# Kernel optimization log

Measured on AMD Instinct MI355X. Metric: run time of the kernel, lower is better.

The kernel has to match this reference:

```python
import jax, jax.numpy as jnp
import numpy as np

HIDDEN_DIM = 2048
HEAD_NUM = 16
HEAD_DIM = HIDDEN_DIM // HEAD_NUM


def setup_inputs() -> dict:
    key = jax.random.key(0)
    ks = jax.random.split(key, 9)
    B, S, H = 2, 2048, HIDDEN_DIM
    scale = 1.0 / np.sqrt(H)
    X = jax.random.normal(ks[0], (B, S, H), dtype=jnp.float32)
    Wq = jax.random.normal(ks[1], (H, H), dtype=jnp.float32) * scale
    bq = jnp.zeros((H,), dtype=jnp.float32)
    Wk = jax.random.normal(ks[2], (H, H), dtype=jnp.float32) * scale
    bk = jnp.zeros((H,), dtype=jnp.float32)
    Wv = jax.random.normal(ks[3], (H, H), dtype=jnp.float32) * scale
    bv = jnp.zeros((H,), dtype=jnp.float32)
    Wo = jax.random.normal(ks[4], (H, H), dtype=jnp.float32) * scale
    bo = jnp.zeros((H,), dtype=jnp.float32)
    return {"X": X, "Wq": Wq, "bq": bq, "Wk": Wk, "bk": bk,
            "Wv": Wv, "bv": bv, "Wo": Wo, "bo": bo}


def reference(X, Wq, bq, Wk, bk, Wv, bv, Wo, bo):
    B, S, H = X.shape
    # QKV projections (nn.Linear applies x @ W.T + b; weights here stored as [in, out])
    Q = X @ Wq + bq
    K = X @ Wk + bk
    V = X @ Wv + bv
    # [B, heads, S, head_dim]
    q = Q.reshape(B, S, HEAD_NUM, HEAD_DIM).transpose(0, 2, 1, 3)
    k = K.reshape(B, S, HEAD_NUM, HEAD_DIM).transpose(0, 2, 1, 3)
    v = V.reshape(B, S, HEAD_NUM, HEAD_DIM).transpose(0, 2, 1, 3)
    scores = jnp.einsum('bhqd,bhkd->bhqk', q, k) / jnp.sqrt(jnp.float32(HEAD_DIM))
    attn = jax.nn.softmax(scores, axis=-1)  # dropout = identity in eval
    out = jnp.einsum('bhqk,bhkd->bhqd', attn, v)
    out = out.transpose(0, 2, 1, 3).reshape(B, S, H)
    return out @ Wo + bo
```

## Files before the change

### kernel.cpp

```cpp
#include <hip/hip_runtime.h>
#include <hip/hip_bf16.h>
#include <stdint.h>


#define Bc 2
#define Sc 2048
#define Hc 2048
#define NHc 16
#define Dc 128
#define Mc 4096

typedef unsigned short ushortT;
typedef float f32x4 __attribute__((ext_vector_type(4)));
typedef _Float16 f16x8 __attribute__((ext_vector_type(8)));

#define MFMAH(a, b, c) __builtin_amdgcn_mfma_f32_16x16x32_f16((a), (b), (c), 0, 0, 0)

static __device__ __forceinline__ ushortT f2h(float x) {
    _Float16 h = (_Float16)x;
    return __builtin_bit_cast(unsigned short, h);
}

static __device__ __forceinline__ void load_lds16(const ushortT* g, ushortT* l) {
    __builtin_amdgcn_global_load_lds(
        (__attribute__((address_space(1))) void*)(g),
        (__attribute__((address_space(3))) void*)(l), 16, 0, 0);
}

__global__ __launch_bounds__(256) void pack_a(
    const float* __restrict__ src, ushortT* __restrict__ dst)
{
    const int mt = blockIdx.x, kt = blockIdx.y;
    const int t = threadIdx.x;
    const int kq = t & 15;
    const int r0 = t >> 4;
    ushortT* tile = dst + ((size_t)(mt * 32 + kt)) * 8192;
#pragma unroll
    for (int rr = 0; rr < 8; ++rr) {
        const int row = r0 + rr * 16;
        const float4 v = *(const float4*)(src + (size_t)(mt * 128 + row) * Hc + kt * 64 + kq * 4);
        _Float16 h[4] = {(_Float16)v.x, (_Float16)v.y, (_Float16)v.z, (_Float16)v.w};
        const int gid = kq >> 1, halfg = kq & 1;
        const int gp = gid ^ (row & 7);
        *(uint2*)(tile + (size_t)row * 64 + gp * 8 + halfg * 4) = *(uint2*)h;
    }
}

__global__ __launch_bounds__(256) void pack_b(
    const float* __restrict__ W0, const float* __restrict__ W1,
    const float* __restrict__ W2, const float* __restrict__ W3,
    ushortT* __restrict__ dst)
{
    const int nt = blockIdx.x, kt = blockIdx.y, which = blockIdx.z;
    const float* W = (which == 0) ? W0 : (which == 1) ? W1 : (which == 2) ? W2 : W3;
    const int t = threadIdx.x;
    const int n = t & 127;
    const int g0 = (t >> 7) * 4;
    ushortT* tile = dst + (size_t)which * 4194304 + ((size_t)(nt * 32 + kt)) * 8192;
#pragma unroll
    for (int gi = 0; gi < 4; ++gi) {
        const int g = g0 + gi;
        _Float16 h[8];
#pragma unroll
        for (int j = 0; j < 8; ++j)
            h[j] = (_Float16)W[(size_t)(kt * 64 + g * 8 + j) * Hc + nt * 128 + n];
        const int gp = g ^ (n & 7);
        *(uint4*)(tile + (size_t)n * 64 + gp * 8) = *(uint4*)h;
    }
}

#define GEMM_PROLOGUE()                                                        \
    __shared__ __align__(16) ushortT As[8192], Bs[8192];                       \
    const int tid = threadIdx.x, wv_ = tid >> 6, lane = tid & 63;              \
    const int lane16 = lane & 15, quad = lane >> 4;                            \
    const int quad4 = quad * 4;                                                \
    const int wm = (wv_ & 1) * 64, wn = (wv_ >> 1) * 64;                       \
    int aoff[4][2], boff[4][2];                                                \
    _Pragma("unroll") for (int mi = 0; mi < 4; ++mi)                           \
        _Pragma("unroll") for (int kf = 0; kf < 2; ++kf) {                     \
            const int ra = wm + mi * 16 + lane16;                              \
            aoff[mi][kf] = ra * 64 + (((kf * 4 + quad) ^ (ra & 7)) << 3);      \
            const int rb = wn + mi * 16 + lane16;                              \
            boff[mi][kf] = rb * 64 + (((kf * 4 + quad) ^ (rb & 7)) << 3);      \
        }                                                                      \
    f32x4 acc[4][4];                                                           \
    _Pragma("unroll") for (int i = 0; i < 4; ++i)                              \
        _Pragma("unroll") for (int j = 0; j < 4; ++j) {                        \
            acc[i][j][0] = 0.f; acc[i][j][1] = 0.f;                            \
            acc[i][j][2] = 0.f; acc[i][j][3] = 0.f; }                          \
    ushortT* asd = &As[wv_ * 2048];                                            \
    ushortT* bsd = &Bs[wv_ * 2048];

#define GEMM_KLOOP(at, bt)                                                     \
    for (int kt2 = 0; kt2 < 32; ++kt2) {                                       \
        _Pragma("unroll") for (int i = 0; i < 4; ++i) {                        \
            load_lds16(at + i * 512 + lane * 8, asd + i * 512);                \
            load_lds16(bt + i * 512 + lane * 8, bsd + i * 512);                \
        }                                                                      \
        at += 8192; bt += 8192;                                                \
        __syncthreads();                                                       \
        _Pragma("unroll") for (int kf = 0; kf < 2; ++kf) {                     \
            f16x8 a[4], b[4];                                                  \
            _Pragma("unroll") for (int mi = 0; mi < 4; ++mi)                   \
                a[mi] = *(const f16x8*)&As[aoff[mi][kf]];                      \
            _Pragma("unroll") for (int nj = 0; nj < 4; ++nj)                   \
                b[nj] = *(const f16x8*)&Bs[boff[nj][kf]];                      \
            _Pragma("unroll") for (int nj = 0; nj < 4; ++nj)                   \
                _Pragma("unroll") for (int mi = 0; mi < 4; ++mi)               \
                    acc[mi][nj] = MFMAH(a[mi], b[nj], acc[mi][nj]);            \
        }                                                                      \
        __syncthreads();                                                       \
    }

__global__ __launch_bounds__(256) void qkv_gemm(
    const ushortT* __restrict__ Xp, const ushortT* __restrict__ Wall,
    const float* __restrict__ bq, const float* __restrict__ bk,
    const float* __restrict__ bv,
    ushortT* __restrict__ Qd, ushortT* __restrict__ Kd, ushortT* __restrict__ Vt)
{
    const int which = blockIdx.x >> 4;
    const int nt = blockIdx.x & 15;
    const int mt = blockIdx.y;
    const ushortT* Wp = Wall + (size_t)which * 4194304;
    const float* bias = (which == 0) ? bq : (which == 1) ? bk : bv;

    GEMM_PROLOGUE();

    const ushortT* at = Xp + (size_t)(mt * 32) * 8192 + wv_ * 2048;
    const ushortT* bt = Wp + (size_t)(nt * 32) * 8192 + wv_ * 2048;
    GEMM_KLOOP(at, bt);

    const float QS = 0.08838834764831845f * 1.4426950408889634f;
#pragma unroll
    for (int nj = 0; nj < 4; ++nj) {
        const int col = nt * 128 + wn + nj * 16 + lane16;
        const float bb = bias[col];
        const int hh = col >> 7, dd = col & 127;
#pragma unroll
        for (int mi = 0; mi < 4; ++mi)
#pragma unroll
            for (int r = 0; r < 4; ++r) {
                const int m = mt * 128 + wm + mi * 16 + quad4 + r;
                const int b = m >> 11, s = m & 2047;
                const float v = acc[mi][nj][r] + bb;
                const size_t bhb = (size_t)(b * NHc + hh) * (Sc * Dc);
                if (which == 0) {
                    Qd[bhb + (size_t)s * Dc + dd] = f2h(v * QS);
                } else if (which == 1) {
                    const int t2 = s >> 6, sin = s & 63;
                    Kd[bhb + (size_t)t2 * 8192 + sin * 128 +
                       (((dd >> 3) ^ (sin & 7)) << 3) + (dd & 7)] = f2h(v);
                } else {
                    const int t2 = s >> 6, sin = s & 63;
                    Vt[bhb + (size_t)t2 * 8192 + dd * 64 +
                       (((sin >> 3) ^ (dd & 7)) << 3) + (sin & 7)] = f2h(v);
                }
            }
    }
}

#define SSTR 68

__global__ __launch_bounds__(256, 2) void attn(
    const ushortT* __restrict__ Qd, const ushortT* __restrict__ Kt,
    const ushortT* __restrict__ Vt, ushortT* __restrict__ AOp)
{
    const int qt = blockIdx.x, hh = blockIdx.y, bb = blockIdx.z;
    const ushortT* Qp  = Qd + ((size_t)(bb * NHc + hh)) * Sc * Dc;
    const ushortT* Kbh = Kt + ((size_t)(bb * NHc + hh)) * Sc * Dc;
    const ushortT* Vbh = Vt + ((size_t)(bb * NHc + hh)) * Sc * Dc;

    __shared__ __align__(16) ushortT Ks[8192];
    __shared__ __align__(16) ushortT Vs[8192];
    __shared__ __align__(16) float   Sbuf[4][16 * SSTR];
    __shared__ __align__(16) ushortT Pbuf[4][1024];
    __shared__ float alphas[4][32], linvs[4][32];

    const int tid = threadIdx.x, wv_ = tid >> 6, lane = tid & 63;
    const int lane16 = lane & 15, quad = lane >> 4;
    const int quad8 = quad * 8, quad4 = quad * 4;
    const int s0 = qt * 128 + wv_ * 32;

    f16x8 q[2][4];
#pragma unroll
    for (int mi = 0; mi < 2; ++mi)
#pragma unroll
        for (int kf = 0; kf < 4; ++kf)
            q[mi][kf] = *(const f16x8*)(Qp + (size_t)(s0 + mi * 16 + lane16) * Dc + kf * 32 + quad8);

    f32x4 o[2][8];
#pragma unroll
    for (int mi = 0; mi < 2; ++mi)
#pragma unroll
        for (int dj = 0; dj < 8; ++dj) { o[mi][dj][0] = 0.f; o[mi][dj][1] = 0.f; o[mi][dj][2] = 0.f; o[mi][dj][3] = 0.f; }

    float m_run[2] = {-1e30f, -1e30f}, l_run[2] = {0.f, 0.f};
    const int srow = lane >> 2;
    const int scol = (lane & 3) * 16;
    float*   Sw = Sbuf[wv_];
    ushortT* Pw = Pbuf[wv_];

    for (int nt = 0; nt < 32; ++nt) {
        const ushortT* ktile = Kbh + (size_t)nt * 8192 + wv_ * 2048;
        const ushortT* vtile = Vbh + (size_t)nt * 8192 + wv_ * 2048;
        ushortT* kdst = Ks + wv_ * 2048;
        ushortT* vdst = Vs + wv_ * 2048;
#pragma unroll
        for (int i = 0; i < 4; ++i) {
            load_lds16(ktile + i * 512 + lane * 8, kdst + i * 512);
            load_lds16(vtile + i * 512 + lane * 8, vdst + i * 512);
        }
        __syncthreads();

        f32x4 sacc[2][4];
#pragma unroll
        for (int mi = 0; mi < 2; ++mi)
#pragma unroll
            for (int nj = 0; nj < 4; ++nj) { sacc[mi][nj][0] = 0.f; sacc[mi][nj][1] = 0.f; sacc[mi][nj][2] = 0.f; sacc[mi][nj][3] = 0.f; }
#pragma unroll
        for (int kf = 0; kf < 4; ++kf) {
            f16x8 kb[4];
#pragma unroll
            for (int nj = 0; nj < 4; ++nj) {
                const int row = nj * 16 + lane16;
                kb[nj] = *(const f16x8*)&Ks[row * 128 + (((kf * 4 + quad) ^ (row & 7)) << 3)];
            }
#pragma unroll
            for (int mi = 0; mi < 2; ++mi)
#pragma unroll
                for (int nj = 0; nj < 4; ++nj)
                    sacc[mi][nj] = MFMAH(q[mi][kf], kb[nj], sacc[mi][nj]);
        }

        f16x8 vb[2][8];
#pragma unroll
        for (int kf2 = 0; kf2 < 2; ++kf2)
#pragma unroll
            for (int dj = 0; dj < 8; ++dj) {
                const int row = dj * 16 + lane16;
                vb[kf2][dj] = *(const f16x8*)&Vs[row * 64 + (((kf2 * 4 + quad) ^ (row & 7)) << 3)];
            }

#pragma unroll
        for (int mi = 0; mi < 2; ++mi) {
#pragma unroll
            for (int nj = 0; nj < 4; ++nj)
#pragma unroll
                for (int r = 0; r < 4; ++r)
                    Sw[(quad4 + r) * SSTR + nj * 16 + lane16] = sacc[mi][nj][r];
            float sv[16];
#pragma unroll
            for (int i = 0; i < 4; ++i)
                *(float4*)&sv[i * 4] = *(const float4*)&Sw[srow * SSTR + scol + i * 4];
            float mx = sv[0];
#pragma unroll
            for (int i = 1; i < 16; ++i) mx = fmaxf(mx, sv[i]);
            mx = fmaxf(mx, __shfl_xor(mx, 1));
            mx = fmaxf(mx, __shfl_xor(mx, 2));
            const float mnew = fmaxf(m_run[mi], mx);
            const float alpha = exp2f(m_run[mi] - mnew);
            m_run[mi] = mnew;
            float sum = 0.f;
#pragma unroll
            for (int i = 0; i < 16; ++i) { const float p = exp2f(sv[i] - mnew); sv[i] = p; sum += p; }
            sum += __shfl_xor(sum, 1);
            sum += __shfl_xor(sum, 2);
            l_run[mi] = l_run[mi] * alpha + sum;
            if ((lane & 3) == 0) alphas[wv_][mi * 16 + srow] = alpha;
            uint32_t pu[8];
#pragma unroll
            for (int i = 0; i < 8; ++i)
                pu[i] = (uint32_t)f2h(sv[2 * i]) | ((uint32_t)f2h(sv[2 * i + 1]) << 16);
#pragma unroll
            for (int j = 0; j < 2; ++j) {
                const int g = (scol >> 3) + j;
                *(uint4*)&Pw[srow * 64 + ((g ^ (srow & 7)) << 3)] = *(uint4*)&pu[j * 4];
            }
#pragma unroll
            for (int r = 0; r < 4; ++r) {
                const float av = alphas[wv_][mi * 16 + quad4 + r];
#pragma unroll
                for (int dj = 0; dj < 8; ++dj) o[mi][dj][r] *= av;
            }
#pragma unroll
            for (int kf2 = 0; kf2 < 2; ++kf2) {
                const f16x8 pa = *(const f16x8*)&Pw[lane16 * 64 + (((kf2 * 4 + quad) ^ (lane16 & 7)) << 3)];
#pragma unroll
                for (int dj = 0; dj < 8; ++dj)
                    o[mi][dj] = MFMAH(pa, vb[kf2][dj], o[mi][dj]);
            }
        }
        __syncthreads();
    }

    if ((lane & 3) == 0) {
        linvs[wv_][srow]      = 1.f / l_run[0];
        linvs[wv_][16 + srow] = 1.f / l_run[1];
    }
#pragma unroll
    for (int mi = 0; mi < 2; ++mi)
#pragma unroll
        for (int r = 0; r < 4; ++r) {
            const int row = mi * 16 + quad4 + r;
            const float li = linvs[wv_][row];
            const int mrow = bb * Sc + qt * 128 + wv_ * 32 + row;
            const int mtile = mrow >> 7, rin = mrow & 127;
#pragma unroll
            for (int dj = 0; dj < 8; ++dj) {
                const int kt2 = hh * 2 + (dj >> 2);
                const int colin = (dj & 3) * 16 + lane16;
                const int g = colin >> 3, e = colin & 7;
                const int gp = g ^ (rin & 7);
                AOp[((size_t)(mtile * 32 + kt2)) * 8192 + rin * 64 + gp * 8 + e] =
                    f2h(o[mi][dj][r] * li);
            }
        }
}

__global__ __launch_bounds__(256) void out_gemm(
    const ushortT* __restrict__ AOp, const ushortT* __restrict__ Wop,
    const float* __restrict__ bo, float* __restrict__ out)
{
    const int nt = blockIdx.x;
    const int mt = blockIdx.y;

    GEMM_PROLOGUE();

    const ushortT* at = AOp + (size_t)(mt * 32) * 8192 + wv_ * 2048;
    const ushortT* bt = Wop + (size_t)(nt * 32) * 8192 + wv_ * 2048;
    GEMM_KLOOP(at, bt);

#pragma unroll
    for (int nj = 0; nj < 4; ++nj) {
        const int col = nt * 128 + wn + nj * 16 + lane16;
        const float bb = bo[col];
#pragma unroll
        for (int mi = 0; mi < 4; ++mi)
#pragma unroll
            for (int r = 0; r < 4; ++r) {
                const int m = mt * 128 + wm + mi * 16 + quad4 + r;
                out[(size_t)m * Hc + col] = acc[mi][nj][r] + bb;
            }
    }
}

extern "C" void kernel_launch(void* const* d_in, const int* in_sizes, int n_in,
                              void* d_out, int out_size, void* d_ws, size_t ws_size,
                              hipStream_t stream) {
    (void)in_sizes; (void)n_in; (void)out_size; (void)ws_size;

    const float* X  = (const float*)d_in[0];
    const float* Wq = (const float*)d_in[1];
    const float* bq = (const float*)d_in[2];
    const float* Wk = (const float*)d_in[3];
    const float* bk = (const float*)d_in[4];
    const float* Wv = (const float*)d_in[5];
    const float* bv = (const float*)d_in[6];
    const float* Wo = (const float*)d_in[7];
    const float* bo = (const float*)d_in[8];
    float* out = (float*)d_out;

    ushortT* ws = (ushortT*)d_ws;
    const size_t E = (size_t)Mc * Hc;
    const size_t WE = (size_t)Hc * Hc;
    ushortT* Xp   = ws;
    ushortT* Wall = Xp + E;
    ushortT* Qd   = Wall + 4 * WE;
    ushortT* Kd   = Qd + E;
    ushortT* Vtp  = Kd + E;
    ushortT* AOp  = Vtp + E;

    pack_a<<<dim3(32, 32), 256, 0, stream>>>(X, Xp);
    pack_b<<<dim3(16, 32, 4), 256, 0, stream>>>(Wq, Wk, Wv, Wo, Wall);
    qkv_gemm<<<dim3(48, 32), 256, 0, stream>>>(Xp, Wall, bq, bk, bv, Qd, Kd, Vtp);
    attn<<<dim3(16, NHc, Bc), 256, 0, stream>>>(Qd, Kd, Vtp, AOp);
    out_gemm<<<dim3(16, 32), 256, 0, stream>>>(AOp, Wall + 3 * WE, bo, out);
}
```

Before: 452.9 us.

## Compute transposed attention scores in registers and drop LDS softmax staging

The attention kernel now computes S^T = K·Q^T and O^T = V^T·P^T with MFMA, so each lane holds a full key column for a query row. Row max and sum then reduce with cross-quad shuffles instead of going through an LDS score buffer, which removes the Sbuf and alphas round-trips. Blocks shrink to 128 threads (64 queries), and a 1D grid is remapped so consecutive blocks cover different heads. This adds K/V reload traffic per query row, since each block now loads full K/V tiles for half as many queries.

```diff
diff --git a/kernel.cpp b/kernel.cpp
--- a/kernel.cpp
+++ b/kernel.cpp
@@ -159,162 +159,157 @@
     }
 }
 
-#define SSTR 68
-
-__global__ __launch_bounds__(256, 2) void attn(
+__global__ __launch_bounds__(128, 2) void attn(
     const ushortT* __restrict__ Qd, const ushortT* __restrict__ Kt,
     const ushortT* __restrict__ Vt, ushortT* __restrict__ AOp)
 {
-    const int qt = blockIdx.x, hh = blockIdx.y, bb = blockIdx.z;
+    const int id = blockIdx.x;
+    const int slot = id >> 3;
+    const int pair = (id & 7) + ((slot >> 5) << 3);
+    const int qt = slot & 31;
+    const int hh = pair & 15, bb = pair >> 4;
+
     const ushortT* Qp  = Qd + ((size_t)(bb * NHc + hh)) * Sc * Dc;
     const ushortT* Kbh = Kt + ((size_t)(bb * NHc + hh)) * Sc * Dc;
     const ushortT* Vbh = Vt + ((size_t)(bb * NHc + hh)) * Sc * Dc;
 
     __shared__ __align__(16) ushortT Ks[8192];
     __shared__ __align__(16) ushortT Vs[8192];
-    __shared__ __align__(16) float   Sbuf[4][16 * SSTR];
-    __shared__ __align__(16) ushortT Pbuf[4][1024];
-    __shared__ float alphas[4][32], linvs[4][32];
+    __shared__ __align__(16) ushortT Pbuf[2][2048];
 
     const int tid = threadIdx.x, wv_ = tid >> 6, lane = tid & 63;
     const int lane16 = lane & 15, quad = lane >> 4;
     const int quad8 = quad * 8, quad4 = quad * 4;
-    const int s0 = qt * 128 + wv_ * 32;
+    const int s0 = qt * 64 + wv_ * 32;
 
     f16x8 q[2][4];
 #pragma unroll
-    for (int mi = 0; mi < 2; ++mi)
+    for (int nj = 0; nj < 2; ++nj)
 #pragma unroll
         for (int kf = 0; kf < 4; ++kf)
-            q[mi][kf] = *(const f16x8*)(Qp + (size_t)(s0 + mi * 16 + lane16) * Dc + kf * 32 + quad8);
-
-    f32x4 o[2][8];
-#pragma unroll
-    for (int mi = 0; mi < 2; ++mi)
-#pragma unroll
-        for (int dj = 0; dj < 8; ++dj) { o[mi][dj][0] = 0.f; o[mi][dj][1] = 0.f; o[mi][dj][2] = 0.f; o[mi][dj][3] = 0.f; }
+            q[nj][kf] = *(const f16x8*)(Qp + (size_t)(s0 + nj * 16 + lane16) * Dc + kf * 32 + quad8);
+
+    f32x4 o[8][2];
+#pragma unroll
+    for (int dj = 0; dj < 8; ++dj)
+#pragma unroll
+        for (int nj = 0; nj < 2; ++nj) { o[dj][nj][0] = 0.f; o[dj][nj][1] = 0.f; o[dj][nj][2] = 0.f; o[dj][nj][3] = 0.f; }
 
     float m_run[2] = {-1e30f, -1e30f}, l_run[2] = {0.f, 0.f};
-    const int srow = lane >> 2;
-    const int scol = (lane & 3) * 16;
-    float*   Sw = Sbuf[wv_];
     ushortT* Pw = Pbuf[wv_];
 
     for (int nt = 0; nt < 32; ++nt) {
-        const ushortT* ktile = Kbh + (size_t)nt * 8192 + wv_ * 2048;
-        const ushortT* vtile = Vbh + (size_t)nt * 8192 + wv_ * 2048;
-        ushortT* kdst = Ks + wv_ * 2048;
-        ushortT* vdst = Vs + wv_ * 2048;
-#pragma unroll
-        for (int i = 0; i < 4; ++i) {
-            load_lds16(ktile + i * 512 + lane * 8, kdst + i * 512);
-            load_lds16(vtile + i * 512 + lane * 8, vdst + i * 512);
+        const ushortT* ktile = Kbh + (size_t)nt * 8192 + wv_ * 4096;
+        const ushortT* vtile = Vbh + (size_t)nt * 8192 + wv_ * 4096;
+#pragma unroll
+        for (int i = 0; i < 8; ++i) {
+            load_lds16(ktile + i * 512 + lane * 8, Ks + wv_ * 4096 + i * 512);
+            load_lds16(vtile + i * 512 + lane * 8, Vs + wv_ * 4096 + i * 512);
         }
         __syncthreads();
 
-        f32x4 sacc[2][4];
-#pragma unroll
-        for (int mi = 0; mi < 2; ++mi)
-#pragma unroll
-            for (int nj = 0; nj < 4; ++nj) { sacc[mi][nj][0] = 0.f; sacc[mi][nj][1] = 0.f; sacc[mi][nj][2] = 0.f; sacc[mi][nj][3] = 0.f; }
+        f32x4 sacc[4][2];
+#pragma unroll
+        for (int mi = 0; mi < 4; ++mi)
+#pragma unroll
+            for (int nj = 0; nj < 2; ++nj) { sacc[mi][nj][0] = 0.f; sacc[mi][nj][1] = 0.f; sacc[mi][nj][2] = 0.f; sacc[mi][nj][3] = 0.f; }
 #pragma unroll
         for (int kf = 0; kf < 4; ++kf) {
             f16x8 kb[4];
 #pragma unroll
-            for (int nj = 0; nj < 4; ++nj) {
+            for (int mi = 0; mi < 4; ++mi) {
+                const int row = mi * 16 + lane16;
+                kb[mi] = *(const f16x8*)&Ks[row * 128 + (((kf * 4 + quad) ^ (row & 7)) << 3)];
+            }
+#pragma unroll
+            for (int mi = 0; mi < 4; ++mi)
+#pragma unroll
+                for (int nj = 0; nj < 2; ++nj)
+                    sacc[mi][nj] = MFMAH(kb[mi], q[nj][kf], sacc[mi][nj]);
+        }
+
+        float alpha_[2];
+#pragma unroll
+        for (int nj = 0; nj < 2; ++nj) {
+            float mx = sacc[0][nj][0];
+#pragma unroll
+            for (int mi = 0; mi < 4; ++mi)
+#pragma unroll
+                for (int r = 0; r < 4; ++r) mx = fmaxf(mx, sacc[mi][nj][r]);
+            mx = fmaxf(mx, __shfl_xor(mx, 16));
+            mx = fmaxf(mx, __shfl_xor(mx, 32));
+            const float mnew = fmaxf(m_run[nj], mx);
+            alpha_[nj] = exp2f(m_run[nj] - mnew);
+            m_run[nj] = mnew;
+            float sum = 0.f;
+#pragma unroll
+            for (int mi = 0; mi < 4; ++mi)
+#pragma unroll
+                for (int r = 0; r < 4; ++r) {
+                    const float p = exp2f(sacc[mi][nj][r] - mnew);
+                    sacc[mi][nj][r] = p;
+                    sum += p;
+                }
+            sum += __shfl_xor(sum, 16);
+            sum += __shfl_xor(sum, 32);
+            l_run[nj] = l_run[nj] * alpha_[nj] + sum;
+            const int prow = nj * 16 + lane16;
+#pragma unroll
+            for (int mi = 0; mi < 4; ++mi) {
+                uint2 u;
+                u.x = (uint32_t)f2h(sacc[mi][nj][0]) | ((uint32_t)f2h(sacc[mi][nj][1]) << 16);
+                u.y = (uint32_t)f2h(sacc[mi][nj][2]) | ((uint32_t)f2h(sacc[mi][nj][3]) << 16);
+                const int g = mi * 2 + (quad >> 1);
+                *(uint2*)&Pw[prow * 64 + ((g ^ (prow & 7)) << 3) + (quad & 1) * 4] = u;
+            }
+        }
+
+#pragma unroll
+        for (int dj = 0; dj < 8; ++dj)
+#pragma unroll
+            for (int nj = 0; nj < 2; ++nj) {
+                const float av = alpha_[nj];
+                o[dj][nj][0] *= av; o[dj][nj][1] *= av;
+                o[dj][nj][2] *= av; o[dj][nj][3] *= av;
+            }
+
+#pragma unroll
+        for (int kf2 = 0; kf2 < 2; ++kf2) {
+            f16x8 pb[2];
+#pragma unroll
+            for (int nj = 0; nj < 2; ++nj) {
                 const int row = nj * 16 + lane16;
-                kb[nj] = *(const f16x8*)&Ks[row * 128 + (((kf * 4 + quad) ^ (row & 7)) << 3)];
-            }
-#pragma unroll
-            for (int mi = 0; mi < 2; ++mi)
-#pragma unroll
-                for (int nj = 0; nj < 4; ++nj)
-                    sacc[mi][nj] = MFMAH(q[mi][kf], kb[nj], sacc[mi][nj]);
-        }
-
-        f16x8 vb[2][8];
-#pragma unroll
-        for (int kf2 = 0; kf2 < 2; ++kf2)
+                pb[nj] = *(const f16x8*)&Pw[row * 64 + (((kf2 * 4 + quad) ^ (row & 7)) << 3)];
+            }
 #pragma unroll
             for (int dj = 0; dj < 8; ++dj) {
                 const int row = dj * 16 + lane16;
-                vb[kf2][dj] = *(const f16x8*)&Vs[row * 64 + (((kf2 * 4 + quad) ^ (row & 7)) << 3)];
-            }
-
-#pragma unroll
-        for (int mi = 0; mi < 2; ++mi) {
-#pragma unroll
-            for (int nj = 0; nj < 4; ++nj)
-#pragma unroll
-                for (int r = 0; r < 4; ++r)
-                    Sw[(quad4 + r) * SSTR + nj * 16 + lane16] = sacc[mi][nj][r];
-            float sv[16];
-#pragma unroll
-            for (int i = 0; i < 4; ++i)
-                *(float4*)&sv[i * 4] = *(const float4*)&Sw[srow * SSTR + scol + i * 4];
-            float mx = sv[0];
-#pragma unroll
-            for (int i = 1; i < 16; ++i) mx = fmaxf(mx, sv[i]);
-            mx = fmaxf(mx, __shfl_xor(mx, 1));
-            mx = fmaxf(mx, __shfl_xor(mx, 2));
-            const float mnew = fmaxf(m_run[mi], mx);
-            const float alpha = exp2f(m_run[mi] - mnew);
-            m_run[mi] = mnew;
-            float sum = 0.f;
-#pragma unroll
-            for (int i = 0; i < 16; ++i) { const float p = exp2f(sv[i] - mnew); sv[i] = p; sum += p; }
-            sum += __shfl_xor(sum, 1);
-            sum += __shfl_xor(sum, 2);
-            l_run[mi] = l_run[mi] * alpha + sum;
-            if ((lane & 3) == 0) alphas[wv_][mi * 16 + srow] = alpha;
-            uint32_t pu[8];
-#pragma unroll
-            for (int i = 0; i < 8; ++i)
-                pu[i] = (uint32_t)f2h(sv[2 * i]) | ((uint32_t)f2h(sv[2 * i + 1]) << 16);
-#pragma unroll
-            for (int j = 0; j < 2; ++j) {
-                const int g = (scol >> 3) + j;
-                *(uint4*)&Pw[srow * 64 + ((g ^ (srow & 7)) << 3)] = *(uint4*)&pu[j * 4];
-            }
-#pragma unroll
-            for (int r = 0; r < 4; ++r) {
-                const float av = alphas[wv_][mi * 16 + quad4 + r];
-#pragma unroll
-                for (int dj = 0; dj < 8; ++dj) o[mi][dj][r] *= av;
-            }
-#pragma unroll
-            for (int kf2 = 0; kf2 < 2; ++kf2) {
-                const f16x8 pa = *(const f16x8*)&Pw[lane16 * 64 + (((kf2 * 4 + quad) ^ (lane16 & 7)) << 3)];
-#pragma unroll
-                for (int dj = 0; dj < 8; ++dj)
-                    o[mi][dj] = MFMAH(pa, vb[kf2][dj], o[mi][dj]);
+                const f16x8 vb = *(const f16x8*)&Vs[row * 64 + (((kf2 * 4 + quad) ^ (row & 7)) << 3)];
+#pragma unroll
+                for (int nj = 0; nj < 2; ++nj)
+                    o[dj][nj] = MFMAH(vb, pb[nj], o[dj][nj]);
             }
         }
         __syncthreads();
     }
 
-    if ((lane & 3) == 0) {
-        linvs[wv_][srow]      = 1.f / l_run[0];
-        linvs[wv_][16 + srow] = 1.f / l_run[1];
-    }
-#pragma unroll
-    for (int mi = 0; mi < 2; ++mi)
-#pragma unroll
-        for (int r = 0; r < 4; ++r) {
-            const int row = mi * 16 + quad4 + r;
-            const float li = linvs[wv_][row];
-            const int mrow = bb * Sc + qt * 128 + wv_ * 32 + row;
-            const int mtile = mrow >> 7, rin = mrow & 127;
-#pragma unroll
-            for (int dj = 0; dj < 8; ++dj) {
-                const int kt2 = hh * 2 + (dj >> 2);
-                const int colin = (dj & 3) * 16 + lane16;
-                const int g = colin >> 3, e = colin & 7;
-                const int gp = g ^ (rin & 7);
-                AOp[((size_t)(mtile * 32 + kt2)) * 8192 + rin * 64 + gp * 8 + e] =
-                    f2h(o[mi][dj][r] * li);
-            }
-        }
+#pragma unroll
+    for (int nj = 0; nj < 2; ++nj) {
+        const float inv = 1.f / l_run[nj];
+        const int m = bb * Sc + qt * 64 + wv_ * 32 + nj * 16 + lane16;
+        const int mtile = m >> 7, rin = m & 127;
+#pragma unroll
+        for (int dj = 0; dj < 8; ++dj) {
+            const int ktile = hh * 2 + (dj >> 2);
+            const int cin0 = (dj & 3) * 16 + quad4;
+            const int g = cin0 >> 3, e0 = cin0 & 7;
+            uint2 u;
+            u.x = (uint32_t)f2h(o[dj][nj][0] * inv) | ((uint32_t)f2h(o[dj][nj][1] * inv) << 16);
+            u.y = (uint32_t)f2h(o[dj][nj][2] * inv) | ((uint32_t)f2h(o[dj][nj][3] * inv) << 16);
+            *(uint2*)&AOp[((size_t)(mtile * 32 + ktile)) * 8192 + rin * 64 +
+                          ((g ^ (rin & 7)) << 3) + e0] = u;
+        }
+    }
 }
 
 __global__ __launch_bounds__(256) void out_gemm(
@@ -373,6 +368,6 @@
     pack_a<<<dim3(32, 32), 256, 0, stream>>>(X, Xp);
     pack_b<<<dim3(16, 32, 4), 256, 0, stream>>>(Wq, Wk, Wv, Wo, Wall);
     qkv_gemm<<<dim3(48, 32), 256, 0, stream>>>(Xp, Wall, bq, bk, bv, Qd, Kd, Vtp);
-    attn<<<dim3(16, NHc, Bc), 256, 0, stream>>>(Qd, Kd, Vtp, AOp);
+    attn<<<dim3(1024), 128, 0, stream>>>(Qd, Kd, Vtp, AOp);
     out_gemm<<<dim3(16, 32), 256, 0, stream>>>(AOp, Wall + 3 * WE, bo, out);
 }
```

Result: no change. 446.6 us (-1.4%).
